# Kernel optimization log

Measured on AMD Instinct MI355X. Metric: run time of the kernel, lower is better.

Reference implementation:

```python
import jax, jax.numpy as jnp
import numpy as np

N_SPANS = 2000
D_SPAN = 1220          # span representation dim (Test_Encoder docstring)
P = 65536              # number of (mention, antecedent) pairs
D_PHI = 60             # dist(20) + genre(20) + speaker(20)
IN_SIZE = 3 * D_SPAN + D_PHI  # 3720
HID = 150
BINS = np.array([1, 2, 3, 4, 5, 8, 16, 32, 64])


def setup_inputs() -> dict:
    key = jax.random.key(0)
    ks = jax.random.split(key, 16)
    inp = {
        "g_i": jax.random.normal(ks[0], (N_SPANS, D_SPAN), dtype=jnp.float32),
        "s_m": jax.random.normal(ks[1], (N_SPANS,), dtype=jnp.float32),
        "mention_ids": jax.random.randint(ks[2], (P,), 0, N_SPANS, dtype=jnp.int32),
        "antecedent_ids": jax.random.randint(ks[3], (P,), 0, N_SPANS, dtype=jnp.int32),
        "distances": jax.random.randint(ks[4], (P,), 1, 512, dtype=jnp.int32),
        "genres": jax.random.randint(ks[5], (P,), 0, 7, dtype=jnp.int32),
        "speakers": jax.random.randint(ks[6], (P,), 0, 3, dtype=jnp.int32),
        # embedding tables
        "dist_emb": jax.random.normal(ks[7], (len(BINS), 20), dtype=jnp.float32) * 0.1,
        "genre_emb": jax.random.normal(ks[8], (7, 20), dtype=jnp.float32) * 0.1,
        "speaker_emb": jax.random.normal(ks[9], (3, 20), dtype=jnp.float32) * 0.1,
        # FFNN params (fc1, fc2, fc3)
        "W1": jax.random.normal(ks[10], (IN_SIZE, HID), dtype=jnp.float32) / np.sqrt(IN_SIZE),
        "b1": jnp.zeros((HID,), dtype=jnp.float32),
        "W2": jax.random.normal(ks[11], (HID, HID), dtype=jnp.float32) / np.sqrt(HID),
        "b2": jnp.zeros((HID,), dtype=jnp.float32),
        "W3": jax.random.normal(ks[12], (HID, 1), dtype=jnp.float32) / np.sqrt(HID),
        "b3": jnp.zeros((1,), dtype=jnp.float32),
    }
    return inp


def _dist_to_bin(distances):
    # replicate Span_Distance_Embedding.dist_to_bin_id: bin id s.t. bins[id] <= d < bins[id+1],
    # last bin catches everything else (including d < 1, per the Python fallthrough).
    bins = jnp.asarray(BINS, dtype=jnp.int32)
    ids = jnp.searchsorted(bins, distances, side="right") - 1
    return jnp.clip(ids, 0, len(BINS) - 1)


def reference(g_i, s_m, mention_ids, antecedent_ids, distances, genres, speakers,
              dist_emb, genre_emb, speaker_emb, W1, b1, W2, b2, W3, b3):
    # phi_ij: concat of distance / genre / speaker embeddings   [P, 60]
    phi = jnp.concatenate(
        [dist_emb[_dist_to_bin(distances)], genre_emb[genres], speaker_emb[speakers]],
        axis=1)
    vec_i = g_i[mention_ids]        # [P, D]
    vec_j = g_i[antecedent_ids]     # [P, D]
    x = jnp.concatenate([vec_i, vec_j, vec_j * vec_j, phi], axis=1)  # [P, 3D+60]
    # FFNN (dropout inactive at eval)
    h = jax.nn.relu(x @ W1 + b1)
    h = jax.nn.relu(h @ W2 + b2)
    s_ij = (h @ W3 + b3)[:, 0]      # [P]
    coref_scores = s_m[mention_ids] + s_m[antecedent_ids] + s_ij
    return coref_scores
```

## Files before the change

### kernel.cpp

```cpp
#include <hip/hip_runtime.h>

typedef short bf16x8 __attribute__((ext_vector_type(8)));
typedef short bf16x4 __attribute__((ext_vector_type(4)));
typedef float f32x4  __attribute__((ext_vector_type(4)));

#define NSPAN 2000
#define DSPAN 1220
#define NPAIR 65536
#define HID   150
#define HP    160
#define TW    320
#define NKS   78
#define NKH   39
#define NMT   128
#define NNT   20
#define KC    6
#define H1S   168

static __device__ __forceinline__ short f2bf(float x) {
  unsigned u = __builtin_bit_cast(unsigned, x);
  u = (u + 0x7FFFu + ((u >> 16) & 1u)) >> 16;
  return (short)u;
}

__global__ __launch_bounds__(256)
void prep_a(const float* __restrict__ g, short* __restrict__ A_fr) {
  int tid = blockIdx.x * 256 + threadIdx.x;
  int l  = tid & 63;
  int t2 = tid >> 6;
  int ks = t2 % NKH;
  int mt = t2 / NKH;
  int m  = mt * 16 + (l & 15);
  int k0 = ks * 32 + ((l >> 4) << 3);
  short v1[8], v2[8];
#pragma unroll
  for (int i = 0; i < 8; ++i) {
    int k = k0 + i;
    float x = (m < NSPAN && k < DSPAN) ? g[m * DSPAN + k] : 0.f;
    v1[i] = f2bf(x);
    v2[i] = f2bf(x * x);
  }
  size_t o1 = ((size_t)(mt * NKS + ks) * 64 + l) * 8;
  *(bf16x8*)(A_fr + o1) = *(const bf16x8*)v1;
  *(bf16x8*)(A_fr + o1 + (size_t)NKH * 512) = *(const bf16x8*)v2;
}

__global__ __launch_bounds__(256)
void prep_weights(const float* __restrict__ W1, const float* __restrict__ b1,
                  const float* __restrict__ de, const float* __restrict__ ge,
                  const float* __restrict__ se, const float* __restrict__ W2,
                  short* __restrict__ Wc_fr, float* __restrict__ phi,
                  short* __restrict__ W2_fr) {
  __shared__ short Lt[320 * 40];
  int b = blockIdx.x;
  int t = threadIdx.x;
  if (b < NKS) {
    int ks = b, k0 = ks * 32;
    for (int idx = t; idx < 32 * 320; idx += 256) {
      int kk = idx / 320;
      int n  = idx - kk * 320;
      int k  = k0 + kk;
      float x = 0.f;
      if (n < HID) {
        if (k < DSPAN) x = W1[k * HID + n];
      } else if (n >= HP && n < HP + HID) {
        int j = n - HP;
        if (k < DSPAN)                   x = W1[(DSPAN + k) * HID + j];
        else if (k >= 1248 && k < 2468)  x = W1[(1192 + k) * HID + j];
      }
      Lt[n * 40 + kk] = f2bf(x);
    }
    __syncthreads();
    int w = t >> 6, l = t & 63;
    int nrow = l & 15, kk8 = (l >> 4) << 3;
#pragma unroll
    for (int i = 0; i < 5; ++i) {
      int nt = w * 5 + i;
      bf16x8 v = *(const bf16x8*)&Lt[(nt * 16 + nrow) * 40 + kk8];
      *(bf16x8*)(Wc_fr + ((size_t)(nt * NKS + ks) * 64 + l) * 8) = v;
    }
  } else if (b < NKS + 13) {
    int idx = (b - NKS) * 256 + t;
    if (idx < 19 * HP) {
      int row = idx / HP;
      int j = idx - row * HP;
      float v = 0.f;
      if (j < HID) {
        const float* emb; int w0;
        if (row < 9)       { emb = de + row * 20;        w0 = 3660; v = b1[j]; }
        else if (row < 16) { emb = ge + (row - 9) * 20;  w0 = 3680; }
        else               { emb = se + (row - 16) * 20; w0 = 3700; }
#pragma unroll
        for (int e = 0; e < 20; ++e) v += emb[e] * W1[(w0 + e) * HID + j];
      }
      phi[idx] = v;
    }
  } else {
    int tid = (b - NKS - 13) * 256 + t;
    if (tid < 3200) {
      int l  = tid & 63;
      int t2 = tid >> 6;
      int ks = t2 % 5;
      int jt = t2 / 5;
      int n  = jt * 16 + (l & 15);
      int k0 = ks * 32 + ((l >> 4) << 3);
      short v[8];
#pragma unroll
      for (int i = 0; i < 8; ++i) {
        int k = k0 + i;
        float x = (k < HID && n < HID) ? W2[k * HID + n] : 0.f;
        v[i] = f2bf(x);
      }
      *(bf16x8*)(W2_fr + (size_t)tid * 8) = *(const bf16x8*)v;
    }
  }
}

__global__ __launch_bounds__(256)
void span_gemm(const short* __restrict__ A_fr, const short* __restrict__ Wc_fr,
               float* __restrict__ T) {
  int t = threadIdx.x, w = t >> 6, l = t & 63;
  int mt  = blockIdx.y * 4 + w;
  int ntb = blockIdx.x * 4;
  int ksb = blockIdx.z * 13;
  const short* pa = A_fr + ((size_t)(mt * NKS + ksb) * 64 + l) * 8;
  const short* pb = Wc_fr + ((size_t)(ntb * NKS + ksb) * 64 + l) * 8;
  f32x4 a0 = {0.f, 0.f, 0.f, 0.f}, a1 = a0, a2 = a0, a3 = a0;
#pragma unroll
  for (int ks = 0; ks < 13; ++ks) {
    bf16x8 a  = *(const bf16x8*)pa;
    bf16x8 b0 = *(const bf16x8*)pb;
    bf16x8 b1 = *(const bf16x8*)(pb + (size_t)NKS * 512);
    bf16x8 b2 = *(const bf16x8*)(pb + (size_t)2 * NKS * 512);
    bf16x8 b3 = *(const bf16x8*)(pb + (size_t)3 * NKS * 512);
    a0 = __builtin_amdgcn_mfma_f32_16x16x32_bf16(a, b0, a0, 0, 0, 0);
    a1 = __builtin_amdgcn_mfma_f32_16x16x32_bf16(a, b1, a1, 0, 0, 0);
    a2 = __builtin_amdgcn_mfma_f32_16x16x32_bf16(a, b2, a2, 0, 0, 0);
    a3 = __builtin_amdgcn_mfma_f32_16x16x32_bf16(a, b3, a3, 0, 0, 0);
    pa += 512; pb += 512;
  }
  int col = l & 15, row4 = (l >> 4) << 2;
  f32x4 acc[4] = {a0, a1, a2, a3};
#pragma unroll
  for (int r = 0; r < 4; ++r) {
    int m = mt * 16 + row4 + r;
    if (m < NSPAN) {
#pragma unroll
      for (int j = 0; j < 4; ++j)
        atomicAdd(&T[m * TW + (ntb + j) * 16 + col], acc[j][r]);
    }
  }
}

__global__ __launch_bounds__(256)
void pair_kernel(const float* __restrict__ T, const float* __restrict__ phi,
                 const short* __restrict__ W2_fr,
                 const float* __restrict__ b2, const float* __restrict__ W3,
                 const float* __restrict__ b3, const float* __restrict__ s_m,
                 const int* __restrict__ m_ids, const int* __restrict__ a_ids,
                 const int* __restrict__ dist, const int* __restrict__ genre,
                 const int* __restrict__ spk, float* __restrict__ out) {
  __shared__ short h1s[64 * H1S];
  __shared__ float w3s[HP], b2s[HP], sm2[64];
  __shared__ int mi[64], ai[64], ob[64], og[64], os[64];

  int t = threadIdx.x;
  int base = blockIdx.x * 64;

  if (t < 64) {
    int p = base + t;
    int m = m_ids[p], a = a_ids[p];
    mi[t] = m; ai[t] = a;
    sm2[t] = s_m[m] + s_m[a];
    int d = dist[p];
    int bb = (d >= 2) + (d >= 3) + (d >= 4) + (d >= 5) + (d >= 8) +
             (d >= 16) + (d >= 32) + (d >= 64);
    ob[t] = bb * HP;
    og[t] = (9 + genre[p]) * HP;
    os[t] = (16 + spk[p]) * HP;
  }
  if (t < HP) {
    w3s[t] = (t < HID) ? W3[t] : 0.f;
    b2s[t] = (t < HID) ? b2[t] : 0.f;
  }
  float b3v = b3[0];
  __syncthreads();

  for (int idx = t; idx < 64 * 40; idx += 256) {
    int p = idx / 40;
    int j = (idx - p * 40) * 4;
    const float4 vm = *(const float4*)&T[mi[p] * TW + j];
    const float4 va = *(const float4*)&T[ai[p] * TW + HP + j];
    const float4 f1 = *(const float4*)&phi[ob[p] + j];
    const float4 f2 = *(const float4*)&phi[og[p] + j];
    const float4 f3 = *(const float4*)&phi[os[p] + j];
    bf16x4 r;
    r[0] = f2bf(fmaxf(vm.x + va.x + f1.x + f2.x + f3.x, 0.f));
    r[1] = f2bf(fmaxf(vm.y + va.y + f1.y + f2.y + f3.y, 0.f));
    r[2] = f2bf(fmaxf(vm.z + va.z + f1.z + f2.z + f3.z, 0.f));
    r[3] = f2bf(fmaxf(vm.w + va.w + f1.w + f2.w + f3.w, 0.f));
    *(bf16x4*)&h1s[p * H1S + j] = r;
  }
  __syncthreads();

  int w = t >> 6, l = t & 63;
  const short* hrow = h1s + (w * 16 + (l & 15)) * H1S + ((l >> 4) << 3);
  bf16x8 af[5];
#pragma unroll
  for (int ks = 0; ks < 5; ++ks) af[ks] = *(const bf16x8*)(hrow + ks * 32);

  f32x4 acc[10];
#pragma unroll
  for (int jt = 0; jt < 10; ++jt) acc[jt] = {0.f, 0.f, 0.f, 0.f};

  const short* pw = W2_fr + l * 8;
#pragma unroll
  for (int jt = 0; jt < 10; ++jt) {
#pragma unroll
    for (int ks = 0; ks < 5; ++ks) {
      bf16x8 bfr = *(const bf16x8*)(pw + (size_t)(jt * 5 + ks) * 512);
      acc[jt] = __builtin_amdgcn_mfma_f32_16x16x32_bf16(af[ks], bfr, acc[jt], 0, 0, 0);
    }
  }

  float part[4] = {0.f, 0.f, 0.f, 0.f};
  int cl = l & 15;
#pragma unroll
  for (int jt = 0; jt < 10; ++jt) {
    int n = jt * 16 + cl;
    float w3v = w3s[n], b2v = b2s[n];
#pragma unroll
    for (int r = 0; r < 4; ++r) part[r] += fmaxf(acc[jt][r] + b2v, 0.f) * w3v;
  }
#pragma unroll
  for (int off = 8; off >= 1; off >>= 1) {
#pragma unroll
    for (int r = 0; r < 4; ++r) part[r] += __shfl_xor(part[r], off, 64);
  }
  if (cl == 0) {
    int rowb = (l >> 4) << 2;
#pragma unroll
    for (int r = 0; r < 4; ++r) {
      int p = w * 16 + rowb + r;
      out[base + p] = sm2[p] + part[r] + b3v;
    }
  }
}

extern "C" void kernel_launch(void* const* d_in, const int* in_sizes, int n_in,
                              void* d_out, int out_size, void* d_ws, size_t ws_size,
                              hipStream_t stream) {
  const float* g     = (const float*)d_in[0];
  const float* s_m   = (const float*)d_in[1];
  const int*   m_ids = (const int*)d_in[2];
  const int*   a_ids = (const int*)d_in[3];
  const int*   dist  = (const int*)d_in[4];
  const int*   genre = (const int*)d_in[5];
  const int*   spk   = (const int*)d_in[6];
  const float* de    = (const float*)d_in[7];
  const float* ge    = (const float*)d_in[8];
  const float* se    = (const float*)d_in[9];
  const float* W1    = (const float*)d_in[10];
  const float* b1    = (const float*)d_in[11];
  const float* W2    = (const float*)d_in[12];
  const float* b2    = (const float*)d_in[13];
  const float* W3    = (const float*)d_in[14];
  const float* b3    = (const float*)d_in[15];
  float* out = (float*)d_out;

  float* T     = (float*)d_ws;
  float* phi   = T + NSPAN * TW;
  short* A_fr  = (short*)(phi + 19 * HP);
  short* Wc_fr = A_fr + (size_t)NMT * NKS * 512;
  short* W2_fr = Wc_fr + (size_t)NNT * NKS * 512;

  hipMemsetAsync(T, 0, NSPAN * TW * sizeof(float), stream);
  prep_a<<<1248, 256, 0, stream>>>(g, A_fr);
  prep_weights<<<NKS + 26, 256, 0, stream>>>(W1, b1, de, ge, se, W2,
                                             Wc_fr, phi, W2_fr);
  span_gemm<<<dim3(5, 32, KC), 256, 0, stream>>>(A_fr, Wc_fr, T);
  pair_kernel<<<NPAIR / 64, 256, 0, stream>>>(T, phi, W2_fr, b2, W3, b3, s_m,
                                              m_ids, a_ids, dist, genre, spk, out);
}
```

Before: 152.0 us.

## Fuse prep kernels and memset, precompute combined phi table per bin/genre/speaker

Merges the memset of T, the span-feature prep and the weight prep into a single prep_all launch, removing two launches and the memset. The W1 fragment packing now writes each fragment directly without an LDS transpose, and g loads are vectorised. The phi embedding contributions are precomputed for all 189 (bin, genre, speaker) combinations, so pair_kernel does one gather per element instead of three. The cost is a larger combo table, some redundant arithmetic in prep, and strided, uncoalesced W1 reads in the new packing path.

After: 126.5 us. 16.7% less time.

```diff
diff --git a/kernel.cpp b/kernel.cpp
--- a/kernel.cpp
+++ b/kernel.cpp
@@ -16,6 +16,13 @@
 #define NNT   20
 #define KC    6
 #define H1S   168
+#define NCMB  189
+
+#define GA 1248
+#define GB 390
+#define GC 119
+#define GD 13
+#define GE 160
 
 static __device__ __forceinline__ short f2bf(float x) {
   unsigned u = __builtin_bit_cast(unsigned, x);
@@ -24,79 +31,90 @@
 }
 
 __global__ __launch_bounds__(256)
-void prep_a(const float* __restrict__ g, short* __restrict__ A_fr) {
-  int tid = blockIdx.x * 256 + threadIdx.x;
-  int l  = tid & 63;
-  int t2 = tid >> 6;
-  int ks = t2 % NKH;
-  int mt = t2 / NKH;
-  int m  = mt * 16 + (l & 15);
-  int k0 = ks * 32 + ((l >> 4) << 3);
-  short v1[8], v2[8];
-#pragma unroll
-  for (int i = 0; i < 8; ++i) {
-    int k = k0 + i;
-    float x = (m < NSPAN && k < DSPAN) ? g[m * DSPAN + k] : 0.f;
-    v1[i] = f2bf(x);
-    v2[i] = f2bf(x * x);
-  }
-  size_t o1 = ((size_t)(mt * NKS + ks) * 64 + l) * 8;
-  *(bf16x8*)(A_fr + o1) = *(const bf16x8*)v1;
-  *(bf16x8*)(A_fr + o1 + (size_t)NKH * 512) = *(const bf16x8*)v2;
-}
-
-__global__ __launch_bounds__(256)
-void prep_weights(const float* __restrict__ W1, const float* __restrict__ b1,
-                  const float* __restrict__ de, const float* __restrict__ ge,
-                  const float* __restrict__ se, const float* __restrict__ W2,
-                  short* __restrict__ Wc_fr, float* __restrict__ phi,
-                  short* __restrict__ W2_fr) {
-  __shared__ short Lt[320 * 40];
+void prep_all(const float* __restrict__ g, const float* __restrict__ W1,
+              const float* __restrict__ b1, const float* __restrict__ de,
+              const float* __restrict__ ge, const float* __restrict__ se,
+              const float* __restrict__ W2, short* __restrict__ A_fr,
+              short* __restrict__ Wc_fr, float* __restrict__ combo,
+              short* __restrict__ W2_fr, float* __restrict__ T) {
   int b = blockIdx.x;
   int t = threadIdx.x;
-  if (b < NKS) {
-    int ks = b, k0 = ks * 32;
-    for (int idx = t; idx < 32 * 320; idx += 256) {
-      int kk = idx / 320;
-      int n  = idx - kk * 320;
-      int k  = k0 + kk;
+  if (b < GA) {
+    int tid = b * 256 + t;
+    int l  = tid & 63;
+    int t2 = tid >> 6;
+    int ks = t2 % NKH;
+    int mt = t2 / NKH;
+    int m  = mt * 16 + (l & 15);
+    int k0 = ks * 32 + ((l >> 4) << 3);
+    float x[8];
+    if (m < NSPAN && k0 + 8 <= DSPAN) {
+      float4 f0 = *(const float4*)&g[m * DSPAN + k0];
+      float4 f1 = *(const float4*)&g[m * DSPAN + k0 + 4];
+      x[0]=f0.x; x[1]=f0.y; x[2]=f0.z; x[3]=f0.w;
+      x[4]=f1.x; x[5]=f1.y; x[6]=f1.z; x[7]=f1.w;
+    } else {
+#pragma unroll
+      for (int i = 0; i < 8; ++i) {
+        int k = k0 + i;
+        x[i] = (m < NSPAN && k < DSPAN) ? g[m * DSPAN + k] : 0.f;
+      }
+    }
+    short v1[8], v2[8];
+#pragma unroll
+    for (int i = 0; i < 8; ++i) { v1[i] = f2bf(x[i]); v2[i] = f2bf(x[i] * x[i]); }
+    size_t o1 = ((size_t)(mt * NKS + ks) * 64 + l) * 8;
+    *(bf16x8*)(A_fr + o1) = *(const bf16x8*)v1;
+    *(bf16x8*)(A_fr + o1 + (size_t)NKH * 512) = *(const bf16x8*)v2;
+  } else if (b < GA + GB) {
+    int tid = (b - GA) * 256 + t;
+    int l  = tid & 63;
+    int t2 = tid >> 6;
+    int ks = t2 % NKS;
+    int nt = t2 / NKS;
+    int n  = nt * 16 + (l & 15);
+    int k0 = ks * 32 + ((l >> 4) << 3);
+    short v[8];
+#pragma unroll
+    for (int i = 0; i < 8; ++i) {
+      int k = k0 + i;
       float x = 0.f;
       if (n < HID) {
-        if (k < DSPAN) x = W1[k * HID + n];
+        if (k < DSPAN)                     x = W1[k * HID + n];
       } else if (n >= HP && n < HP + HID) {
         int j = n - HP;
-        if (k < DSPAN)                   x = W1[(DSPAN + k) * HID + j];
-        else if (k >= 1248 && k < 2468)  x = W1[(1192 + k) * HID + j];
+        if (k < DSPAN)                     x = W1[(DSPAN + k) * HID + j];
+        else if (k >= 1248 && k < 2468)    x = W1[(1192 + k) * HID + j];
       }
-      Lt[n * 40 + kk] = f2bf(x);
-    }
-    __syncthreads();
-    int w = t >> 6, l = t & 63;
-    int nrow = l & 15, kk8 = (l >> 4) << 3;
-#pragma unroll
-    for (int i = 0; i < 5; ++i) {
-      int nt = w * 5 + i;
-      bf16x8 v = *(const bf16x8*)&Lt[(nt * 16 + nrow) * 40 + kk8];
-      *(bf16x8*)(Wc_fr + ((size_t)(nt * NKS + ks) * 64 + l) * 8) = v;
-    }
-  } else if (b < NKS + 13) {
-    int idx = (b - NKS) * 256 + t;
-    if (idx < 19 * HP) {
-      int row = idx / HP;
-      int j = idx - row * HP;
+      v[i] = f2bf(x);
+    }
+    *(bf16x8*)(Wc_fr + (size_t)tid * 8) = *(const bf16x8*)v;
+  } else if (b < GA + GB + GC) {
+    int idx = (b - GA - GB) * 256 + t;
+    if (idx < NCMB * HP) {
+      int c = idx / HP;
+      int j = idx - c * HP;
       float v = 0.f;
       if (j < HID) {
-        const float* emb; int w0;
-        if (row < 9)       { emb = de + row * 20;        w0 = 3660; v = b1[j]; }
-        else if (row < 16) { emb = ge + (row - 9) * 20;  w0 = 3680; }
-        else               { emb = se + (row - 16) * 20; w0 = 3700; }
-#pragma unroll
-        for (int e = 0; e < 20; ++e) v += emb[e] * W1[(w0 + e) * HID + j];
+        int si = c % 3;
+        int t2 = c / 3;
+        int gi = t2 % 7;
+        int bi = t2 / 7;
+        v = b1[j];
+        const float* dp = de + bi * 20;
+        const float* gp = ge + gi * 20;
+        const float* sp = se + si * 20;
+#pragma unroll
+        for (int e = 0; e < 20; ++e) {
+          v += dp[e] * W1[(3660 + e) * HID + j];
+          v += gp[e] * W1[(3680 + e) * HID + j];
+          v += sp[e] * W1[(3700 + e) * HID + j];
+        }
       }
-      phi[idx] = v;
-    }
-  } else {
-    int tid = (b - NKS - 13) * 256 + t;
+      combo[idx] = v;
+    }
+  } else if (b < GA + GB + GC + GD) {
+    int tid = (b - GA - GB - GC) * 256 + t;
     if (tid < 3200) {
       int l  = tid & 63;
       int t2 = tid >> 6;
@@ -113,6 +131,10 @@
       }
       *(bf16x8*)(W2_fr + (size_t)tid * 8) = *(const bf16x8*)v;
     }
+  } else {
+    int idx = (b - GA - GB - GC - GD) * 256 + t;
+    f32x4 z = {0.f, 0.f, 0.f, 0.f};
+    if (idx < NSPAN * TW / 4) ((f32x4*)T)[idx] = z;
   }
 }
 
@@ -153,7 +175,7 @@
 }
 
 __global__ __launch_bounds__(256)
-void pair_kernel(const float* __restrict__ T, const float* __restrict__ phi,
+void pair_kernel(const float* __restrict__ T, const float* __restrict__ combo,
                  const short* __restrict__ W2_fr,
                  const float* __restrict__ b2, const float* __restrict__ W3,
                  const float* __restrict__ b3, const float* __restrict__ s_m,
@@ -162,7 +184,7 @@
                  const int* __restrict__ spk, float* __restrict__ out) {
   __shared__ short h1s[64 * H1S];
   __shared__ float w3s[HP], b2s[HP], sm2[64];
-  __shared__ int mi[64], ai[64], ob[64], og[64], os[64];
+  __shared__ int mi[64], ai[64], co[64];
 
   int t = threadIdx.x;
   int base = blockIdx.x * 64;
@@ -175,9 +197,7 @@
     int d = dist[p];
     int bb = (d >= 2) + (d >= 3) + (d >= 4) + (d >= 5) + (d >= 8) +
              (d >= 16) + (d >= 32) + (d >= 64);
-    ob[t] = bb * HP;
-    og[t] = (9 + genre[p]) * HP;
-    os[t] = (16 + spk[p]) * HP;
+    co[t] = ((bb * 7 + genre[p]) * 3 + spk[p]) * HP;
   }
   if (t < HP) {
     w3s[t] = (t < HID) ? W3[t] : 0.f;
@@ -191,14 +211,12 @@
     int j = (idx - p * 40) * 4;
     const float4 vm = *(const float4*)&T[mi[p] * TW + j];
     const float4 va = *(const float4*)&T[ai[p] * TW + HP + j];
-    const float4 f1 = *(const float4*)&phi[ob[p] + j];
-    const float4 f2 = *(const float4*)&phi[og[p] + j];
-    const float4 f3 = *(const float4*)&phi[os[p] + j];
+    const float4 fc = *(const float4*)&combo[co[p] + j];
     bf16x4 r;
-    r[0] = f2bf(fmaxf(vm.x + va.x + f1.x + f2.x + f3.x, 0.f));
-    r[1] = f2bf(fmaxf(vm.y + va.y + f1.y + f2.y + f3.y, 0.f));
-    r[2] = f2bf(fmaxf(vm.z + va.z + f1.z + f2.z + f3.z, 0.f));
-    r[3] = f2bf(fmaxf(vm.w + va.w + f1.w + f2.w + f3.w, 0.f));
+    r[0] = f2bf(fmaxf(vm.x + va.x + fc.x, 0.f));
+    r[1] = f2bf(fmaxf(vm.y + va.y + fc.y, 0.f));
+    r[2] = f2bf(fmaxf(vm.z + va.z + fc.z, 0.f));
+    r[3] = f2bf(fmaxf(vm.w + va.w + fc.w, 0.f));
     *(bf16x4*)&h1s[p * H1S + j] = r;
   }
   __syncthreads();
@@ -269,16 +287,14 @@
   float* out = (float*)d_out;
 
   float* T     = (float*)d_ws;
-  float* phi   = T + NSPAN * TW;
-  short* A_fr  = (short*)(phi + 19 * HP);
+  float* combo = T + NSPAN * TW;
+  short* A_fr  = (short*)(combo + NCMB * HP);
   short* Wc_fr = A_fr + (size_t)NMT * NKS * 512;
   short* W2_fr = Wc_fr + (size_t)NNT * NKS * 512;
 
-  hipMemsetAsync(T, 0, NSPAN * TW * sizeof(float), stream);
-  prep_a<<<1248, 256, 0, stream>>>(g, A_fr);
-  prep_weights<<<NKS + 26, 256, 0, stream>>>(W1, b1, de, ge, se, W2,
-                                             Wc_fr, phi, W2_fr);
+  prep_all<<<GA + GB + GC + GD + GE, 256, 0, stream>>>(
+      g, W1, b1, de, ge, se, W2, A_fr, Wc_fr, combo, W2_fr, T);
   span_gemm<<<dim3(5, 32, KC), 256, 0, stream>>>(A_fr, Wc_fr, T);
-  pair_kernel<<<NPAIR / 64, 256, 0, stream>>>(T, phi, W2_fr, b2, W3, b3, s_m,
+  pair_kernel<<<NPAIR / 64, 256, 0, stream>>>(T, combo, W2_fr, b2, W3, b3, s_m,
                                               m_ids, a_ids, dist, genre, spk, out);
 }
```
